# Kernel tuning notes

Hardware: AMD Instinct MI355X
Metric: run time of the kernel (lower is better)

## Reference

```python
import jax, jax.numpy as jnp
import numpy as np

B, T, E, H = 1024, 200, 128, 128
N_ITEMS, N_CATS = 100000, 1000
LN_EPS = 1e-5


def _prelu(x, a):
    return jnp.where(x >= 0, x, a * x)


def _layernorm(x, g, b):
    m = x.mean(-1, keepdims=True)
    v = ((x - m) ** 2).mean(-1, keepdims=True)
    return (x - m) / jnp.sqrt(v + LN_EPS) * g + b


def setup_inputs() -> dict:
    key = jax.random.key(0)
    it = iter(jax.random.split(key, 64))
    nx = lambda: next(it)
    def lin(out_d, in_d):
        s = 1.0 / np.sqrt(in_d)
        return jax.random.uniform(nx(), (out_d, in_d), jnp.float32, -s, s)
    inp = {}
    inp['behavior_ids'] = jax.random.randint(nx(), (B, T), 0, N_ITEMS)
    inp['candidate_id'] = jax.random.randint(nx(), (B,), 0, N_ITEMS)
    inp['candidate_cat'] = jax.random.randint(nx(), (B,), 0, N_CATS)
    inp['dense_features'] = jax.random.normal(nx(), (B, 5), jnp.float32)
    inp['item_emb'] = (jax.random.normal(nx(), (N_ITEMS, E), jnp.float32) * 0.01).at[0].set(0.0)
    inp['cat_emb'] = (jax.random.normal(nx(), (N_CATS, E // 2), jnp.float32) * 0.01).at[0].set(0.0)
    # nn.GRU params (gate order r,z,n)
    inp['gru_wih'] = lin(3 * H, E)
    inp['gru_whh'] = lin(3 * H, H)
    inp['gru_bih'] = jnp.zeros((3 * H,), jnp.float32)
    inp['gru_bhh'] = jnp.zeros((3 * H,), jnp.float32)
    # auxiliary_net: Linear(H,E) -> ReLU -> Linear(E,1)
    inp['aux_w1'] = lin(E, H); inp['aux_b1'] = jnp.zeros((E,), jnp.float32)
    inp['aux_w2'] = lin(1, E); inp['aux_b2'] = jnp.zeros((1,), jnp.float32)
    # attention_mlp: Linear(3H,64) -> PReLU -> Linear(64,1)
    inp['att_w1'] = lin(64, 3 * H); inp['att_b1'] = jnp.zeros((64,), jnp.float32)
    inp['att_a'] = jnp.array(0.25, jnp.float32)
    inp['att_w2'] = lin(1, 64); inp['att_b2'] = jnp.zeros((1,), jnp.float32)
    # AUGRU gates: Linear(2H, H) each
    inp['wz'] = lin(H, 2 * H); inp['bz'] = jnp.zeros((H,), jnp.float32)
    inp['wr'] = lin(H, 2 * H); inp['br'] = jnp.zeros((H,), jnp.float32)
    inp['wh'] = lin(H, 2 * H); inp['bh'] = jnp.zeros((H,), jnp.float32)
    # dense_proj Linear(5,32)
    inp['dp_w'] = lin(32, 5); inp['dp_b'] = jnp.zeros((32,), jnp.float32)
    # MLP: 352 -> 256 -> 128 -> 64, each Linear + LayerNorm + PReLU
    dims = [H + E + E // 2 + 32, 256, 128, 64]
    for i in range(3):
        inp[f'm_w{i+1}'] = lin(dims[i + 1], dims[i])
        inp[f'm_b{i+1}'] = jnp.zeros((dims[i + 1],), jnp.float32)
        inp[f'ln_g{i+1}'] = jnp.ones((dims[i + 1],), jnp.float32)
        inp[f'ln_b{i+1}'] = jnp.zeros((dims[i + 1],), jnp.float32)
        inp[f'pa{i+1}'] = jnp.array(0.25, jnp.float32)
    # 3 task heads Linear(64,1), stacked
    inp['heads_w'] = lin(3, 64); inp['heads_b'] = jnp.zeros((3,), jnp.float32)
    return inp


def _forward_core(behavior_ids, candidate_id, candidate_cat, dense_features,
                  item_emb, cat_emb, gru_wih, gru_whh, gru_bih, gru_bhh,
                  aux_w1, aux_b1, aux_w2, aux_b2,
                  att_w1, att_b1, att_a, att_w2, att_b2,
                  wz, bz, wr, br, wh, bh, dp_w, dp_b,
                  m_w1, m_b1, ln_g1, ln_b1, pa1,
                  m_w2, m_b2, ln_g2, ln_b2, pa2,
                  m_w3, m_b3, ln_g3, ln_b3, pa3,
                  heads_w, heads_b):
    beh = item_emb[behavior_ids]            # [B,T,E]
    cand = item_emb[candidate_id]           # [B,E]
    catv = cat_emb[candidate_cat]           # [B,E//2]
    Bsz = beh.shape[0]
    Hd = gru_whh.shape[1]
    h0 = jnp.zeros((Bsz, Hd), beh.dtype)
    # --- interest extractor GRU (cuDNN GRU math, gate order r,z,n) ---
    xp = jnp.einsum('bte,ge->btg', beh, gru_wih) + gru_bih  # [B,T,3H]
    def gru_step(h, x):
        hp = h @ gru_whh.T + gru_bhh
        xr, xz, xn = jnp.split(x, 3, -1)
        hr, hz, hn = jnp.split(hp, 3, -1)
        r = jax.nn.sigmoid(xr + hr)
        z = jax.nn.sigmoid(xz + hz)
        n = jnp.tanh(xn + r * hn)
        hnew = (1 - z) * n + z * h
        return hnew, hnew
    _, hs = jax.lax.scan(gru_step, h0, jnp.swapaxes(xp, 0, 1))
    hs = jnp.swapaxes(hs, 0, 1)             # [B,T,H]
    # --- auxiliary logits ---
    aux = jax.nn.relu(hs[:, :-1] @ aux_w1.T + aux_b1) @ aux_w2.T + aux_b2  # [B,T-1,1]
    # --- attention (embed_dim == hidden_size so cand_proj == candidate_emb) ---
    ce = cand[:, None, :]
    att_in = jnp.concatenate([hs, jnp.broadcast_to(ce, hs.shape), hs * ce], -1)  # [B,T,3H]
    scores = (_prelu(att_in @ att_w1.T + att_b1, att_a) @ att_w2.T + att_b2)[..., 0]
    att = jax.nn.softmax(scores, axis=-1)   # [B,T]
    # --- AUGRU: attention-modulated update gate ---
    def augru_step(h, xs):
        x, a = xs                           # x: [B,H], a: [B]
        comb = jnp.concatenate([x, h], -1)
        z = jax.nn.sigmoid(comb @ wz.T + bz)
        r = jax.nn.sigmoid(comb @ wr.T + br)
        comb_r = jnp.concatenate([x, r * h], -1)
        ht = jnp.tanh(comb_r @ wh.T + bh)
        zp = a[:, None] * z
        return (1 - zp) * h + zp * ht, None
    hT, _ = jax.lax.scan(augru_step, h0, (jnp.swapaxes(hs, 0, 1), att.T))
    # --- fusion MLP (dropout is identity in eval) ---
    dense_out = dense_features @ dp_w.T + dp_b
    x = jnp.concatenate([hT, cand, catv, dense_out], -1)  # [B,352]
    for (w, b, g, be, a) in ((m_w1, m_b1, ln_g1, ln_b1, pa1),
                             (m_w2, m_b2, ln_g2, ln_b2, pa2),
                             (m_w3, m_b3, ln_g3, ln_b3, pa3)):
        x = _prelu(_layernorm(x @ w.T + b, g, be), a)
    preds = jax.nn.sigmoid(x @ heads_w.T + heads_b)  # [B,3] == 3 heads of [B,1]
    return preds, aux


def reference(behavior_ids, candidate_id, candidate_cat, dense_features,
              item_emb, cat_emb, gru_wih, gru_whh, gru_bih, gru_bhh,
              aux_w1, aux_b1, aux_w2, aux_b2,
              att_w1, att_b1, att_a, att_w2, att_b2,
              wz, bz, wr, br, wh, bh, dp_w, dp_b,
              m_w1, m_b1, ln_g1, ln_b1, pa1,
              m_w2, m_b2, ln_g2, ln_b2, pa2,
              m_w3, m_b3, ln_g3, ln_b3, pa3,
              heads_w, heads_b):
    return _forward_core(behavior_ids, candidate_id, candidate_cat, dense_features,
                         item_emb, cat_emb, gru_wih, gru_whh, gru_bih, gru_bhh,
                         aux_w1, aux_b1, aux_w2, aux_b2,
                         att_w1, att_b1, att_a, att_w2, att_b2,
                         wz, bz, wr, br, wh, bh, dp_w, dp_b,
                         m_w1, m_b1, ln_g1, ln_b1, pa1,
                         m_w2, m_b2, ln_g2, ln_b2, pa2,
                         m_w3, m_b3, ln_g3, ln_b3, pa3,
                         heads_w, heads_b)
```

## Files before the change

kernel.cpp:

```cpp
#include <hip/hip_runtime.h>


typedef __bf16 bf16;
typedef float f32x4 __attribute__((ext_vector_type(4)));
typedef __bf16 bf16x8 __attribute__((ext_vector_type(8)));
typedef __bf16 bf16x4 __attribute__((ext_vector_type(4)));

#define MFMA16(a, b, c) __builtin_amdgcn_mfma_f32_16x16x32_bf16((a), (b), (c), 0, 0, 0)

#define BATCH 1024
#define SEQT 200
#define F32_ONE 0x3F800000u

__device__ __forceinline__ float sigm(float x) {
  return __builtin_amdgcn_rcpf(1.0f + __expf(-x));
}
__device__ __forceinline__ float tanh_fast(float x) {
  float ax = fabsf(x);
  float t = 1.0f - 2.0f * __builtin_amdgcn_rcpf(__expf(2.0f * ax) + 1.0f);
  return copysignf(t, x);
}

__device__ __forceinline__ void bar_lgkm() {
  asm volatile("s_waitcnt lgkmcnt(0)\n\ts_barrier" ::: "memory");
}

__device__ __forceinline__ void dma16(const void* g, void* l) {
  __builtin_amdgcn_global_load_lds((__attribute__((address_space(1))) void*)g,
                                   (__attribute__((address_space(3))) void*)l,
                                   16, 0, 0);
}

template <typename DT> __device__ __forceinline__ float ldf(const DT* p, long i);
template <> __device__ __forceinline__ float ldf<bf16>(const bf16* p, long i) { return (float)p[i]; }
template <> __device__ __forceinline__ float ldf<float>(const float* p, long i) { return p[i]; }

template <typename DT> __device__ __forceinline__ bf16x8 ld8(const DT* p, long i);
template <> __device__ __forceinline__ bf16x8 ld8<bf16>(const bf16* p, long i) {
  return *(const bf16x8*)(p + i);
}
template <> __device__ __forceinline__ bf16x8 ld8<float>(const float* p, long i) {
  f32x4 a = *(const f32x4*)(p + i);
  f32x4 b = *(const f32x4*)(p + i + 4);
  bf16x8 r;
  r[0] = (bf16)a[0]; r[1] = (bf16)a[1]; r[2] = (bf16)a[2]; r[3] = (bf16)a[3];
  r[4] = (bf16)b[0]; r[5] = (bf16)b[1]; r[6] = (bf16)b[2]; r[7] = (bf16)b[3];
  return r;
}

template <typename DT>
__device__ __forceinline__ void prep_body(
    const int* __restrict__ cid, const int* __restrict__ ccat,
    const DT* __restrict__ dense, const DT* __restrict__ item_emb,
    const DT* __restrict__ cat_emb, const DT* __restrict__ dp_w,
    const DT* __restrict__ dp_b, bf16* __restrict__ candbuf, bf16* __restrict__ xf) {
  const int b = blockIdx.x;
  const int t = threadIdx.x;
  bf16 v = (bf16)ldf(item_emb, (long)cid[b] * 128 + t);
  candbuf[b * 128 + t] = v;
  xf[(long)b * 352 + 128 + t] = v;
  if (t < 64) xf[(long)b * 352 + 256 + t] = (bf16)ldf(cat_emb, (long)ccat[b] * 64 + t);
  if (t < 32) {
    float s = ldf(dp_b, t);
    for (int k = 0; k < 5; k++) s += ldf(dense, b * 5 + k) * ldf(dp_w, t * 5 + k);
    xf[(long)b * 352 + 320 + t] = (bf16)s;
  }
}
__global__ __launch_bounds__(128) void k_prep(
    const unsigned* __restrict__ disc, const int* cid, const int* ccat,
    const void* dense, const void* item_emb, const void* cat_emb,
    const void* dp_w, const void* dp_b, bf16* candbuf, bf16* xf) {
  if (*disc == F32_ONE)
    prep_body<float>(cid, ccat, (const float*)dense, (const float*)item_emb,
                     (const float*)cat_emb, (const float*)dp_w, (const float*)dp_b, candbuf, xf);
  else
    prep_body<bf16>(cid, ccat, (const bf16*)dense, (const bf16*)item_emb,
                    (const bf16*)cat_emb, (const bf16*)dp_w, (const bf16*)dp_b, candbuf, xf);
}

template <typename DT>
__device__ __forceinline__ void gru3_body(
    const int* __restrict__ ids, const DT* __restrict__ item_emb,
    const DT* __restrict__ wih, const DT* __restrict__ whh,
    const DT* __restrict__ bih, const DT* __restrict__ bhh, bf16* __restrict__ hs,
    bf16 (*hA)[16][136], bf16 (*xb)[4][16][136], char* raw) {
  const int b0 = blockIdx.x * 16;
  const int tid = threadIdx.x;
  const int w = tid >> 6, lane = tid & 63, l15 = lane & 15, quad = lane >> 4;
  const int nc = w * 16 + l15;

  for (int i = tid; i < 2 * 16 * 136; i += 512) ((bf16*)hA)[i] = (bf16)0.0f;

  bf16x8 wir[4], wiz[4], win_[4], whr[4], whz[4], whn[4];
#pragma unroll
  for (int k = 0; k < 4; k++) {
    const long off = k * 32 + quad * 8;
    wir[k] = ld8(wih, (long)nc * 128 + off);
    wiz[k] = ld8(wih, (long)(128 + nc) * 128 + off);
    win_[k] = ld8(wih, (long)(256 + nc) * 128 + off);
    whr[k] = ld8(whh, (long)nc * 128 + off);
    whz[k] = ld8(whh, (long)(128 + nc) * 128 + off);
    whn[k] = ld8(whh, (long)(256 + nc) * 128 + off);
  }
  const float br_s = ldf(bih, nc) + ldf(bhh, nc);
  const float bz_s = ldf(bih, 128 + nc) + ldf(bhh, 128 + nc);
  const float bxn_s = ldf(bih, 256 + nc);
  const float bhn_s = ldf(bhh, 256 + nc);

  const int idrow = (sizeof(DT) == 4) ? (tid >> 5) : ((tid >> 4) & 15);
  const int* idbase = ids + (long)(b0 + idrow) * SEQT;

  auto DMA = [&](const int4 id4) {
    if constexpr (sizeof(DT) == 4) {
#pragma unroll
      for (int j = 0; j < 4; j++)
        dma16((const char*)(item_emb + (long)((&id4.x)[j]) * 128) + (tid & 31) * 16,
              raw + (j * 512 + tid) * 16);
    } else {
#pragma unroll
      for (int j = 0; j < 2; j++) {
        const int slot = j * 2 + (tid >> 8);
        dma16((const char*)(item_emb + (long)((&id4.x)[slot]) * 128) + (tid & 15) * 16,
              raw + (j * 512 + tid) * 16);
      }
    }
  };
  auto CONV = [&](int buf) {
    if constexpr (sizeof(DT) == 4) {
      const float* rf = (const float*)raw;
#pragma unroll
      for (int h = 0; h < 4; h++) {
        const int e = h * 2048 + tid * 4;
        f32x4 a = *(const f32x4*)(rf + e);
        const int slot = e >> 11, row = (e >> 7) & 15, col = e & 127;
        bf16x4 o;
        o[0] = (bf16)a[0]; o[1] = (bf16)a[1]; o[2] = (bf16)a[2]; o[3] = (bf16)a[3];
        *(bf16x4*)&xb[buf][slot][row][col] = o;
      }
    } else {
      const bf16* rh = (const bf16*)raw;
#pragma unroll
      for (int h = 0; h < 2; h++) {
        const int e = h * 4096 + tid * 8;
        const int slot = e >> 11, row = (e >> 7) & 15, col = e & 127;
        *(bf16x8*)&xb[buf][slot][row][col] = *(const bf16x8*)(rh + e);
      }
    }
  };

  const int srow = tid >> 5, sch = (tid & 31) * 4;
  bf16* hsb = hs + ((long)(b0 + srow) * SEQT) * 128 + sch;

  float hreg[4] = {0.f, 0.f, 0.f, 0.f};
  const f32x4 z4 = {0.f, 0.f, 0.f, 0.f};

  int4 idv = *(const int4*)(idbase);
  DMA(idv);
  idv = *(const int4*)(idbase + 4);
  asm volatile("s_waitcnt vmcnt(1)" ::: "memory");
  __builtin_amdgcn_sched_barrier(0);
  __builtin_amdgcn_s_barrier();
  CONV(0);
  asm volatile("s_waitcnt lgkmcnt(0)" ::: "memory");
  __builtin_amdgcn_sched_barrier(0);
  __builtin_amdgcn_s_barrier();
  DMA(idv);
  idv = *(const int4*)(idbase + 8);

#define GRU_STEP(P, S)                                                         \
  {                                                                            \
    const int tt = t0 + (S);                                                   \
    bf16x8 af[4], xaf[4];                                                      \
    _Pragma("unroll") for (int k = 0; k < 4; k++) {                            \
      af[k] = *(const bf16x8*)&hA[P][l15][k * 32 + quad * 8];                  \
      xaf[k] = *(const bf16x8*)&xb[buf][S][l15][k * 32 + quad * 8];            \
    }                                                                          \
    { const int slot = tt ? tt - 1 : 0;                                        \
      bf16x4 hv = *(const bf16x4*)&hA[P][srow][sch];                           \
      *(bf16x4*)(hsb + (long)slot * 128) = hv; }                               \
    f32x4 ar = z4, az = z4, axn = z4, ahn = z4;                                \
    _Pragma("unroll") for (int k = 0; k < 4; k++) {                            \
      ar = MFMA16(xaf[k], wir[k], ar);                                         \
      az = MFMA16(xaf[k], wiz[k], az);                                         \
      axn = MFMA16(xaf[k], win_[k], axn);                                      \
    }                                                                          \
    _Pragma("unroll") for (int k = 0; k < 4; k++) {                            \
      ar = MFMA16(af[k], whr[k], ar);                                          \
      az = MFMA16(af[k], whz[k], az);                                          \
      ahn = MFMA16(af[k], whn[k], ahn);                                        \
    }                                                                          \
    _Pragma("unroll") for (int r = 0; r < 4; r++) {                            \
      float r_ = sigm(ar[r] + br_s);                                           \
      float z_ = sigm(az[r] + bz_s);                                           \
      float n_ = tanh_fast(axn[r] + bxn_s + r_ * (ahn[r] + bhn_s));            \
      float hnew = (1.0f - z_) * n_ + z_ * hreg[r];                            \
      hreg[r] = hnew;                                                          \
      hA[(P) ^ 1][quad * 4 + r][nc] = (bf16)hnew;                              \
    }                                                                          \
    bar_lgkm();                                                                \
  }

  for (int c = 0; c < 50; c++) {
    const int t0 = c * 4;
    const int buf = c & 1;
    GRU_STEP(0, 0) GRU_STEP(1, 1) GRU_STEP(0, 2) GRU_STEP(1, 3)
    if (c < 49) {
      asm volatile("s_waitcnt vmcnt(4)" ::: "memory");
      __builtin_amdgcn_sched_barrier(0);
      __builtin_amdgcn_s_barrier();
      CONV((c + 1) & 1);
      asm volatile("s_waitcnt lgkmcnt(0)" ::: "memory");
      __builtin_amdgcn_sched_barrier(0);
      __builtin_amdgcn_s_barrier();
      if (c < 48) {
        DMA(idv);
        int nid = (c + 3) * 4; if (nid > 196) nid = 196;
        idv = *(const int4*)(idbase + nid);
      }
    }
  }
#undef GRU_STEP
  { bf16x4 hv = *(const bf16x4*)&hA[0][srow][sch];
    *(bf16x4*)(hsb + (long)(SEQT - 1) * 128) = hv; }
}
__global__ __launch_bounds__(512, 1) void k_gru3(
    const unsigned* __restrict__ disc, const int* ids, const void* item_emb,
    const void* wih, const void* whh, const void* bih, const void* bhh, bf16* hs) {
  __shared__ __align__(16) bf16 hA[2][16][136];
  __shared__ __align__(16) bf16 xb[2][4][16][136];
  __shared__ __align__(16) char raw[32768];
  if (*disc == F32_ONE)
    gru3_body<float>(ids, (const float*)item_emb, (const float*)wih, (const float*)whh,
                     (const float*)bih, (const float*)bhh, hs, hA, xb, raw);
  else
    gru3_body<bf16>(ids, (const bf16*)item_emb, (const bf16*)wih, (const bf16*)whh,
                    (const bf16*)bih, (const bf16*)bhh, hs, hA, xb, raw);
}

template <typename DT>
__device__ __forceinline__ void augru3_body(
    const bf16* __restrict__ hsrc, const float* __restrict__ att,
    const DT* __restrict__ wz, const DT* __restrict__ wr, const DT* __restrict__ wh,
    const DT* __restrict__ bzv, const DT* __restrict__ brv, const DT* __restrict__ bhv,
    bf16* __restrict__ xf_out,
    bf16 (*hA)[16][136], bf16 (*rhA)[136], float (*attL)[201],
    bf16 (*xb)[4][16][136], char* raw) {
  const int b0 = blockIdx.x * 16;
  const int tid = threadIdx.x;
  const int w = tid >> 6, lane = tid & 63, l15 = lane & 15, quad = lane >> 4;
  const int nc = w * 16 + l15;

  for (int i = tid; i < 2 * 16 * 136; i += 512) ((bf16*)hA)[i] = (bf16)0.0f;
  for (int i = tid; i < 16 * SEQT; i += 512) {
    int r = i / SEQT, c = i - r * SEQT;
    attL[r][c] = att[(long)(b0 + r) * SEQT + c];
  }

  bf16x8 wzx[4], wzh[4], wrx[4], wrh[4], whx[4], whh_[4];
#pragma unroll
  for (int k = 0; k < 4; k++) {
    const long off = k * 32 + quad * 8;
    wzx[k] = ld8(wz, (long)nc * 256 + off);
    wzh[k] = ld8(wz, (long)nc * 256 + 128 + off);
    wrx[k] = ld8(wr, (long)nc * 256 + off);
    wrh[k] = ld8(wr, (long)nc * 256 + 128 + off);
    whx[k] = ld8(wh, (long)nc * 256 + off);
    whh_[k] = ld8(wh, (long)nc * 256 + 128 + off);
  }
  const float bz_s = ldf(bzv, nc);
  const float br_s = ldf(brv, nc);
  const float bh_s = ldf(bhv, nc);

  auto DMA = [&](int t0) {
#pragma unroll
    for (int j = 0; j < 2; j++) {
      const int slot = j * 2 + (tid >> 8);
      const int row = (tid >> 4) & 15;
      const bf16* src = hsrc + ((long)(b0 + row) * SEQT + t0 + slot) * 128 + (tid & 15) * 8;
      dma16(src, raw + (j * 512 + tid) * 16);
    }
  };
  auto CONV = [&](int buf) {
    const bf16* rh = (const bf16*)raw;
#pragma unroll
    for (int h = 0; h < 2; h++) {
      const int e = h * 4096 + tid * 8;
      const int slot = e >> 11, row = (e >> 7) & 15, col = e & 127;
      *(bf16x8*)&xb[buf][slot][row][col] = *(const bf16x8*)(rh + e);
    }
  };

  float hreg[4] = {0.f, 0.f, 0.f, 0.f};
  const f32x4 z4 = {0.f, 0.f, 0.f, 0.f};

  DMA(0);
  asm volatile("s_waitcnt vmcnt(0)" ::: "memory");
  __builtin_amdgcn_sched_barrier(0);
  __builtin_amdgcn_s_barrier();
  CONV(0);
  asm volatile("s_waitcnt lgkmcnt(0)" ::: "memory");
  __builtin_amdgcn_sched_barrier(0);
  __builtin_amdgcn_s_barrier();
  DMA(4);

#define AUGRU_STEP(P, S)                                                       \
  {                                                                            \
    const int tt = t0 + (S);                                                   \
    bf16x8 af[4], xaf[4];                                                      \
    _Pragma("unroll") for (int k = 0; k < 4; k++) {                            \
      af[k] = *(const bf16x8*)&hA[P][l15][k * 32 + quad * 8];                  \
      xaf[k] = *(const bf16x8*)&xb[buf][S][l15][k * 32 + quad * 8];            \
    }                                                                          \
    f32x4 az = z4, ar = z4, axh = z4;                                          \
    _Pragma("unroll") for (int k = 0; k < 4; k++) {                            \
      az = MFMA16(xaf[k], wzx[k], az);                                         \
      ar = MFMA16(xaf[k], wrx[k], ar);                                         \
      axh = MFMA16(xaf[k], whx[k], axh);                                       \
    }                                                                          \
    _Pragma("unroll") for (int k = 0; k < 4; k++) {                            \
      az = MFMA16(af[k], wzh[k], az);                                          \
      ar = MFMA16(af[k], wrh[k], ar);                                          \
    }                                                                          \
    float zp[4];                                                               \
    _Pragma("unroll") for (int r = 0; r < 4; r++) {                            \
      float a_ = attL[quad * 4 + r][tt];                                       \
      float z_ = sigm(az[r] + bz_s);                                           \
      float r_ = sigm(ar[r] + br_s);                                           \
      zp[r] = a_ * z_;                                                         \
      rhA[quad * 4 + r][nc] = (bf16)(r_ * hreg[r]);                            \
    }                                                                          \
    bar_lgkm();                                                                \
    bf16x8 rf[4];                                                              \
    _Pragma("unroll") for (int k = 0; k < 4; k++)                              \
      rf[k] = *(const bf16x8*)&rhA[l15][k * 32 + quad * 8];                    \
    f32x4 ahh = axh;                                                           \
    _Pragma("unroll") for (int k = 0; k < 4; k++)                              \
      ahh = MFMA16(rf[k], whh_[k], ahh);                                       \
    _Pragma("unroll") for (int r = 0; r < 4; r++) {                            \
      float ht = tanh_fast(ahh[r] + bh_s);                                     \
      float hnew = (1.f - zp[r]) * hreg[r] + zp[r] * ht;                       \
      hreg[r] = hnew;                                                          \
      hA[(P) ^ 1][quad * 4 + r][nc] = (bf16)hnew;                              \
    }                                                                          \
    bar_lgkm();                                                                \
  }

  for (int c = 0; c < 50; c++) {
    const int t0 = c * 4;
    const int buf = c & 1;
    AUGRU_STEP(0, 0) AUGRU_STEP(1, 1) AUGRU_STEP(0, 2) AUGRU_STEP(1, 3)
    if (c < 49) {
      asm volatile("s_waitcnt vmcnt(0)" ::: "memory");
      __builtin_amdgcn_sched_barrier(0);
      __builtin_amdgcn_s_barrier();
      CONV((c + 1) & 1);
      asm volatile("s_waitcnt lgkmcnt(0)" ::: "memory");
      __builtin_amdgcn_sched_barrier(0);
      __builtin_amdgcn_s_barrier();
      if (c < 48) DMA((c + 2) * 4);
    }
  }
#undef AUGRU_STEP
#pragma unroll
  for (int r = 0; r < 4; r++)
    xf_out[(long)(b0 + quad * 4 + r) * 352 + nc] = (bf16)hreg[r];
}
__global__ __launch_bounds__(512, 1) void k_augru3(
    const unsigned* __restrict__ disc, const bf16* hsrc, const float* att,
    const void* wz, const void* wr, const void* wh,
    const void* bzv, const void* brv, const void* bhv, bf16* xf_out) {
  __shared__ __align__(16) bf16 hA[2][16][136];
  __shared__ __align__(16) bf16 rhA[16][136];
  __shared__ __align__(16) float attL[16][201];
  __shared__ __align__(16) bf16 xb[2][4][16][136];
  __shared__ __align__(16) char raw[16384];
  if (*disc == F32_ONE)
    augru3_body<float>(hsrc, att, (const float*)wz, (const float*)wr, (const float*)wh,
                       (const float*)bzv, (const float*)brv, (const float*)bhv, xf_out,
                       hA, rhA, attL, xb, raw);
  else
    augru3_body<bf16>(hsrc, att, (const bf16*)wz, (const bf16*)wr, (const bf16*)wh,
                      (const bf16*)bzv, (const bf16*)brv, (const bf16*)bhv, xf_out,
                      hA, rhA, attL, xb, raw);
}

template <typename DT>
__device__ __forceinline__ void aux_body(
    const bf16* __restrict__ hs, const DT* __restrict__ w1, const DT* __restrict__ b1v,
    const DT* __restrict__ w2v, const DT* __restrict__ b2v, float* __restrict__ outaux,
    bf16 (*As)[136], bf16 (*Ws)[136]) {
  const int bg = blockIdx.y;
  const int t0 = blockIdx.x * 64;
  const int tid = threadIdx.x;
  const int w = tid >> 6, lane = tid & 63, l15 = lane & 15, quad = lane >> 4;
#pragma unroll
  for (int j = 0; j < 8; j++) {
    int ci = j * 256 + tid;
    int row = ci >> 4, k8 = (ci & 15) * 8;
    *(bf16x8*)&Ws[row][k8] = ld8(w1, (long)row * 128 + k8);
  }
  float b1c[8], w2c[8];
#pragma unroll
  for (int nt = 0; nt < 8; nt++) {
    int n = nt * 16 + l15;
    b1c[nt] = ldf(b1v, n);
    w2c[nt] = ldf(w2v, n);
  }
  const float b2 = ldf(b2v, 0);
  const f32x4 z4 = {0.f, 0.f, 0.f, 0.f};
  __syncthreads();

  for (int bi = 0; bi < 16; bi++) {
    const int b = bg * 16 + bi;
#pragma unroll
    for (int j = 0; j < 4; j++) {
      int ci = j * 256 + tid;
      int row = ci >> 4, k8 = (ci & 15) * 8;
      int t = t0 + row; int tc = t < 199 ? t : 198;
      *(bf16x8*)&As[row][k8] = *(const bf16x8*)(hs + ((long)b * SEQT + tc) * 128 + k8);
    }
    bar_lgkm();
    bf16x8 af[4];
#pragma unroll
    for (int k = 0; k < 4; k++) af[k] = *(const bf16x8*)&As[w * 16 + l15][k * 32 + quad * 8];
    float part[4] = {0.f, 0.f, 0.f, 0.f};
#pragma unroll
    for (int nt = 0; nt < 8; nt++) {
      f32x4 acc = z4;
#pragma unroll
      for (int k = 0; k < 4; k++) {
        bf16x8 bfr = *(const bf16x8*)&Ws[nt * 16 + l15][k * 32 + quad * 8];
        acc = MFMA16(af[k], bfr, acc);
      }
#pragma unroll
      for (int r = 0; r < 4; r++) {
        float y = acc[r] + b1c[nt];
        part[r] += (y > 0.f ? y : 0.f) * w2c[nt];
      }
    }
#pragma unroll
    for (int m = 1; m < 16; m <<= 1)
#pragma unroll
      for (int r = 0; r < 4; r++) part[r] += __shfl_xor(part[r], m, 64);
    if (l15 == 0) {
#pragma unroll
      for (int r = 0; r < 4; r++) {
        int t = t0 + w * 16 + quad * 4 + r;
        if (t < 199) outaux[(long)b * 199 + t] = part[r] + b2;
      }
    }
    bar_lgkm();
  }
}
__global__ __launch_bounds__(256) void k_aux(
    const unsigned* __restrict__ disc, const bf16* hs, const void* w1, const void* b1v,
    const void* w2v, const void* b2v, float* outaux) {
  __shared__ bf16 As[64][136];
  __shared__ bf16 Ws[128][136];
  if (*disc == F32_ONE)
    aux_body<float>(hs, (const float*)w1, (const float*)b1v, (const float*)w2v,
                    (const float*)b2v, outaux, As, Ws);
  else
    aux_body<bf16>(hs, (const bf16*)w1, (const bf16*)b1v, (const bf16*)w2v,
                   (const bf16*)b2v, outaux, As, Ws);
}

template <typename DT>
__device__ __forceinline__ void att_body(
    const bf16* __restrict__ hs, const bf16* __restrict__ cand,
    const DT* __restrict__ w1, const DT* __restrict__ b1v, const DT* __restrict__ a_s,
    const DT* __restrict__ w2v, const DT* __restrict__ b2v, float* __restrict__ scores,
    bf16 (*As)[392], bf16 (*Ws)[392]) {
  const int bg = blockIdx.y;
  const int t0 = blockIdx.x * 64;
  const int tid = threadIdx.x;
  const int w = tid >> 6, lane = tid & 63, l15 = lane & 15, quad = lane >> 4;
#pragma unroll
  for (int j = 0; j < 12; j++) {
    int ci = j * 256 + tid;
    int row = ci / 48;
    int k8 = (ci % 48) * 8;
    *(bf16x8*)&Ws[row][k8] = ld8(w1, (long)row * 384 + k8);
  }
  const float aP = ldf(a_s, 0);
  const float b2 = ldf(b2v, 0);
  float b1c[4], w2c[4];
#pragma unroll
  for (int nt = 0; nt < 4; nt++) {
    int n = nt * 16 + l15;
    b1c[nt] = ldf(b1v, n);
    w2c[nt] = ldf(w2v, n);
  }
  const f32x4 z4 = {0.f, 0.f, 0.f, 0.f};
  __syncthreads();

  for (int bi = 0; bi < 16; bi++) {
    const int b = bg * 16 + bi;
#pragma unroll
    for (int j = 0; j < 12; j++) {
      int ci = j * 256 + tid;
      int row = ci / 48;
      int k8 = (ci % 48) * 8;
      int t = t0 + row; int tc = t < SEQT ? t : SEQT - 1;
      const bf16* hrow = hs + ((long)b * SEQT + tc) * 128;
      bf16x8 v;
      if (k8 < 128) v = *(const bf16x8*)(hrow + k8);
      else if (k8 < 256) v = *(const bf16x8*)(cand + b * 128 + (k8 - 128));
      else {
        bf16x8 hv = *(const bf16x8*)(hrow + (k8 - 256));
        bf16x8 cv = *(const bf16x8*)(cand + b * 128 + (k8 - 256));
#pragma unroll
        for (int q = 0; q < 8; q++) v[q] = (bf16)((float)hv[q] * (float)cv[q]);
      }
      *(bf16x8*)&As[row][k8] = v;
    }
    bar_lgkm();
    f32x4 acc[4] = {z4, z4, z4, z4};
    for (int k = 0; k < 12; k++) {
      bf16x8 af = *(const bf16x8*)&As[w * 16 + l15][k * 32 + quad * 8];
#pragma unroll
      for (int nt = 0; nt < 4; nt++) {
        bf16x8 bfr = *(const bf16x8*)&Ws[nt * 16 + l15][k * 32 + quad * 8];
        acc[nt] = MFMA16(af, bfr, acc[nt]);
      }
    }
    float part[4] = {0.f, 0.f, 0.f, 0.f};
#pragma unroll
    for (int nt = 0; nt < 4; nt++) {
#pragma unroll
      for (int r = 0; r < 4; r++) {
        float y = acc[nt][r] + b1c[nt];
        y = (y >= 0.f) ? y : aP * y;
        part[r] += y * w2c[nt];
      }
    }
#pragma unroll
    for (int m = 1; m < 16; m <<= 1)
#pragma unroll
      for (int r = 0; r < 4; r++) part[r] += __shfl_xor(part[r], m, 64);
    if (l15 == 0) {
#pragma unroll
      for (int r = 0; r < 4; r++) {
        int t = t0 + w * 16 + quad * 4 + r;
        if (t < SEQT) scores[(long)b * SEQT + t] = part[r] + b2;
      }
    }
    bar_lgkm();
  }
}
__global__ __launch_bounds__(256) void k_att(
    const unsigned* __restrict__ disc, const bf16* hs, const bf16* cand,
    const void* w1, const void* b1v, const void* a_s,
    const void* w2v, const void* b2v, float* scores) {
  __shared__ bf16 As[64][392];
  __shared__ bf16 Ws[64][392];
  if (*disc == F32_ONE)
    att_body<float>(hs, cand, (const float*)w1, (const float*)b1v, (const float*)a_s,
                    (const float*)w2v, (const float*)b2v, scores, As, Ws);
  else
    att_body<bf16>(hs, cand, (const bf16*)w1, (const bf16*)b1v, (const bf16*)a_s,
                   (const bf16*)w2v, (const bf16*)b2v, scores, As, Ws);
}

__global__ __launch_bounds__(256) void k_softmax(float* __restrict__ sc) {
  const int b = blockIdx.x, tid = threadIdx.x;
  __shared__ float red[256];
  float v = (tid < SEQT) ? sc[(long)b * SEQT + tid] : -1e30f;
  red[tid] = v; __syncthreads();
  for (int s = 128; s > 0; s >>= 1) { if (tid < s) red[tid] = fmaxf(red[tid], red[tid + s]); __syncthreads(); }
  float mx = red[0]; __syncthreads();
  float e = (tid < SEQT) ? __expf(v - mx) : 0.f;
  red[tid] = e; __syncthreads();
  for (int s = 128; s > 0; s >>= 1) { if (tid < s) red[tid] += red[tid + s]; __syncthreads(); }
  float inv = 1.0f / red[0];
  if (tid < SEQT) sc[(long)b * SEQT + tid] = e * inv;
}

template <typename DT>
__device__ __forceinline__ void mlp_body(
    const bf16* __restrict__ xf,
    const DT* __restrict__ w1, const DT* __restrict__ b1, const DT* __restrict__ g1, const DT* __restrict__ be1, const DT* __restrict__ pa1,
    const DT* __restrict__ w2, const DT* __restrict__ b2, const DT* __restrict__ g2, const DT* __restrict__ be2, const DT* __restrict__ pa2,
    const DT* __restrict__ w3, const DT* __restrict__ b3, const DT* __restrict__ g3, const DT* __restrict__ be3, const DT* __restrict__ pa3,
    const DT* __restrict__ hw, const DT* __restrict__ hb, float* __restrict__ preds,
    float (*xs)[352], float (*ys)[256]) {
  const int tid = threadIdx.x, w = tid >> 6, lane = tid & 63;
  const int b = blockIdx.x * 4 + w;
  for (int i = lane; i < 352; i += 64) xs[w][i] = (float)xf[(long)b * 352 + i];
  __syncthreads();
  float acc1[4];
#pragma unroll
  for (int oi = 0; oi < 4; oi++) {
    int o = lane + 64 * oi;
    float s = ldf(b1, o);
    for (int k = 0; k < 352; k += 8) {
      bf16x8 wv = ld8(w1, (long)o * 352 + k);
#pragma unroll
      for (int j = 0; j < 8; j++) s += xs[w][k + j] * (float)wv[j];
    }
    acc1[oi] = s;
  }
  float sm = acc1[0] + acc1[1] + acc1[2] + acc1[3];
#pragma unroll
  for (int m = 1; m < 64; m <<= 1) sm += __shfl_xor(sm, m, 64);
  float mean = sm * (1.0f / 256.0f);
  float vs = 0.f;
#pragma unroll
  for (int oi = 0; oi < 4; oi++) { float d = acc1[oi] - mean; vs += d * d; }
#pragma unroll
  for (int m = 1; m < 64; m <<= 1) vs += __shfl_xor(vs, m, 64);
  float rstd = rsqrtf(vs * (1.0f / 256.0f) + 1e-5f);
  float a1 = ldf(pa1, 0);
#pragma unroll
  for (int oi = 0; oi < 4; oi++) {
    int o = lane + 64 * oi;
    float y = (acc1[oi] - mean) * rstd * ldf(g1, o) + ldf(be1, o);
    ys[w][o] = (y >= 0.f) ? y : a1 * y;
  }
  __syncthreads();
  float acc2[2];
#pragma unroll
  for (int oi = 0; oi < 2; oi++) {
    int o = lane + 64 * oi;
    float s = ldf(b2, o);
    for (int k = 0; k < 256; k += 8) {
      bf16x8 wv = ld8(w2, (long)o * 256 + k);
#pragma unroll
      for (int j = 0; j < 8; j++) s += ys[w][k + j] * (float)wv[j];
    }
    acc2[oi] = s;
  }
  sm = acc2[0] + acc2[1];
#pragma unroll
  for (int m = 1; m < 64; m <<= 1) sm += __shfl_xor(sm, m, 64);
  mean = sm * (1.0f / 128.0f);
  vs = 0.f;
#pragma unroll
  for (int oi = 0; oi < 2; oi++) { float d = acc2[oi] - mean; vs += d * d; }
#pragma unroll
  for (int m = 1; m < 64; m <<= 1) vs += __shfl_xor(vs, m, 64);
  rstd = rsqrtf(vs * (1.0f / 128.0f) + 1e-5f);
  float a2 = ldf(pa2, 0);
  __syncthreads();
#pragma unroll
  for (int oi = 0; oi < 2; oi++) {
    int o = lane + 64 * oi;
    float y = (acc2[oi] - mean) * rstd * ldf(g2, o) + ldf(be2, o);
    xs[w][o] = (y >= 0.f) ? y : a2 * y;
  }
  __syncthreads();
  float s3 = ldf(b3, lane);
  for (int k = 0; k < 128; k += 8) {
    bf16x8 wv = ld8(w3, (long)lane * 128 + k);
#pragma unroll
    for (int j = 0; j < 8; j++) s3 += xs[w][k + j] * (float)wv[j];
  }
  sm = s3;
#pragma unroll
  for (int m = 1; m < 64; m <<= 1) sm += __shfl_xor(sm, m, 64);
  mean = sm * (1.0f / 64.0f);
  float d3 = s3 - mean;
  vs = d3 * d3;
#pragma unroll
  for (int m = 1; m < 64; m <<= 1) vs += __shfl_xor(vs, m, 64);
  rstd = rsqrtf(vs * (1.0f / 64.0f) + 1e-5f);
  float a3 = ldf(pa3, 0);
  float y3 = d3 * rstd * ldf(g3, lane) + ldf(be3, lane);
  y3 = (y3 >= 0.f) ? y3 : a3 * y3;
  ys[w][lane] = y3;
  __syncthreads();
  if (lane < 3) {
    float s = ldf(hb, lane);
    for (int k = 0; k < 64; k++) s += ys[w][k] * ldf(hw, lane * 64 + k);
    preds[(long)b * 3 + lane] = sigm(s);
  }
}
__global__ __launch_bounds__(256) void k_mlp(
    const unsigned* __restrict__ disc, const bf16* xf,
    const void* w1, const void* b1, const void* g1, const void* be1, const void* pa1,
    const void* w2, const void* b2, const void* g2, const void* be2, const void* pa2,
    const void* w3, const void* b3, const void* g3, const void* be3, const void* pa3,
    const void* hw, const void* hb, float* preds) {
  __shared__ float xs[4][352];
  __shared__ float ys[4][256];
  if (*disc == F32_ONE)
    mlp_body<float>(xf,
        (const float*)w1, (const float*)b1, (const float*)g1, (const float*)be1, (const float*)pa1,
        (const float*)w2, (const float*)b2, (const float*)g2, (const float*)be2, (const float*)pa2,
        (const float*)w3, (const float*)b3, (const float*)g3, (const float*)be3, (const float*)pa3,
        (const float*)hw, (const float*)hb, preds, xs, ys);
  else
    mlp_body<bf16>(xf,
        (const bf16*)w1, (const bf16*)b1, (const bf16*)g1, (const bf16*)be1, (const bf16*)pa1,
        (const bf16*)w2, (const bf16*)b2, (const bf16*)g2, (const bf16*)be2, (const bf16*)pa2,
        (const bf16*)w3, (const bf16*)b3, (const bf16*)g3, (const bf16*)be3, (const bf16*)pa3,
        (const bf16*)hw, (const bf16*)hb, preds, xs, ys);
}

extern "C" void kernel_launch(void* const* d_in, const int* in_sizes, int n_in,
                              void* d_out, int out_size, void* d_ws, size_t ws_size,
                              hipStream_t stream) {
  const int* behavior_ids = (const int*)d_in[0];
  const int* candidate_id = (const int*)d_in[1];
  const int* candidate_cat = (const int*)d_in[2];
  const void* dense = d_in[3];
  const void* item_emb = d_in[4];
  const void* cat_emb = d_in[5];
  const void* gru_wih = d_in[6];
  const void* gru_whh = d_in[7];
  const void* gru_bih = d_in[8];
  const void* gru_bhh = d_in[9];
  const void* aux_w1 = d_in[10];
  const void* aux_b1 = d_in[11];
  const void* aux_w2 = d_in[12];
  const void* aux_b2 = d_in[13];
  const void* att_w1 = d_in[14];
  const void* att_b1 = d_in[15];
  const void* att_a = d_in[16];
  const void* att_w2 = d_in[17];
  const void* att_b2 = d_in[18];
  const void* wz = d_in[19];
  const void* bz = d_in[20];
  const void* wr = d_in[21];
  const void* br = d_in[22];
  const void* wh = d_in[23];
  const void* bh = d_in[24];
  const void* dp_w = d_in[25];
  const void* dp_b = d_in[26];
  const void* m_w1 = d_in[27];
  const void* m_b1 = d_in[28];
  const void* ln_g1 = d_in[29];
  const void* ln_b1 = d_in[30];
  const void* pa1 = d_in[31];
  const void* m_w2 = d_in[32];
  const void* m_b2 = d_in[33];
  const void* ln_g2 = d_in[34];
  const void* ln_b2 = d_in[35];
  const void* pa2 = d_in[36];
  const void* m_w3 = d_in[37];
  const void* m_b3 = d_in[38];
  const void* ln_g3 = d_in[39];
  const void* ln_b3 = d_in[40];
  const void* pa3 = d_in[41];
  const void* heads_w = d_in[42];
  const void* heads_b = d_in[43];
  (void)in_sizes; (void)n_in; (void)out_size; (void)ws_size;

  const unsigned* disc = (const unsigned*)ln_g1;

  char* ws = (char*)d_ws;
  bf16* HS = (bf16*)(ws);
  float* SC = (float*)(ws + 52428800L);
  bf16* CAND = (bf16*)(ws + 53248000L);
  bf16* XF = (bf16*)(ws + 53510144L);
  float* OUT = (float*)d_out;

  k_prep<<<BATCH, 128, 0, stream>>>(disc, candidate_id, candidate_cat, dense, item_emb,
                                    cat_emb, dp_w, dp_b, CAND, XF);
  k_gru3<<<64, 512, 0, stream>>>(disc, behavior_ids, item_emb, gru_wih, gru_whh,
                                 gru_bih, gru_bhh, HS);
  k_aux<<<dim3(4, 64), 256, 0, stream>>>(disc, HS, aux_w1, aux_b1, aux_w2, aux_b2, OUT + 3072);
  k_att<<<dim3(4, 64), 256, 0, stream>>>(disc, HS, CAND, att_w1, att_b1, att_a, att_w2, att_b2, SC);
  k_softmax<<<BATCH, 256, 0, stream>>>(SC);
  k_augru3<<<64, 512, 0, stream>>>(disc, HS, SC, wz, wr, wh, bz, br, bh, XF);
  k_mlp<<<256, 256, 0, stream>>>(disc, XF,
      m_w1, m_b1, ln_g1, ln_b1, pa1,
      m_w2, m_b2, ln_g2, ln_b2, pa2,
      m_w3, m_b3, ln_g3, ln_b3, pa3,
      heads_w, heads_b, OUT);
}
```

Before: 831.4 us.

## Fuse prep, aux, attention and softmax into one heads kernel

```diff
diff --git a/kernel.cpp b/kernel.cpp
--- a/kernel.cpp
+++ b/kernel.cpp
@@ -46,36 +46,6 @@
   r[0] = (bf16)a[0]; r[1] = (bf16)a[1]; r[2] = (bf16)a[2]; r[3] = (bf16)a[3];
   r[4] = (bf16)b[0]; r[5] = (bf16)b[1]; r[6] = (bf16)b[2]; r[7] = (bf16)b[3];
   return r;
-}
-
-template <typename DT>
-__device__ __forceinline__ void prep_body(
-    const int* __restrict__ cid, const int* __restrict__ ccat,
-    const DT* __restrict__ dense, const DT* __restrict__ item_emb,
-    const DT* __restrict__ cat_emb, const DT* __restrict__ dp_w,
-    const DT* __restrict__ dp_b, bf16* __restrict__ candbuf, bf16* __restrict__ xf) {
-  const int b = blockIdx.x;
-  const int t = threadIdx.x;
-  bf16 v = (bf16)ldf(item_emb, (long)cid[b] * 128 + t);
-  candbuf[b * 128 + t] = v;
-  xf[(long)b * 352 + 128 + t] = v;
-  if (t < 64) xf[(long)b * 352 + 256 + t] = (bf16)ldf(cat_emb, (long)ccat[b] * 64 + t);
-  if (t < 32) {
-    float s = ldf(dp_b, t);
-    for (int k = 0; k < 5; k++) s += ldf(dense, b * 5 + k) * ldf(dp_w, t * 5 + k);
-    xf[(long)b * 352 + 320 + t] = (bf16)s;
-  }
-}
-__global__ __launch_bounds__(128) void k_prep(
-    const unsigned* __restrict__ disc, const int* cid, const int* ccat,
-    const void* dense, const void* item_emb, const void* cat_emb,
-    const void* dp_w, const void* dp_b, bf16* candbuf, bf16* xf) {
-  if (*disc == F32_ONE)
-    prep_body<float>(cid, ccat, (const float*)dense, (const float*)item_emb,
-                     (const float*)cat_emb, (const float*)dp_w, (const float*)dp_b, candbuf, xf);
-  else
-    prep_body<bf16>(cid, ccat, (const bf16*)dense, (const bf16*)item_emb,
-                    (const bf16*)cat_emb, (const bf16*)dp_w, (const bf16*)dp_b, candbuf, xf);
 }
 
 template <typename DT>
@@ -238,6 +208,165 @@
 }
 
 template <typename DT>
+__device__ __forceinline__ void heads_body(
+    const bf16* __restrict__ hs,
+    const int* __restrict__ cid, const int* __restrict__ ccat,
+    const DT* __restrict__ dense, const DT* __restrict__ item_emb,
+    const DT* __restrict__ cat_emb, const DT* __restrict__ dp_w, const DT* __restrict__ dp_b,
+    const DT* __restrict__ aw1, const DT* __restrict__ ab1,
+    const DT* __restrict__ aw2, const DT* __restrict__ ab2,
+    const DT* __restrict__ tw1, const DT* __restrict__ tb1, const DT* __restrict__ ta,
+    const DT* __restrict__ tw2, const DT* __restrict__ tb2,
+    float* __restrict__ sc, float* __restrict__ outaux, bf16* __restrict__ xf,
+    bf16 (*Wt)[392], bf16 (*Wa)[136], float (*scL)[208]) {
+  const int bg = blockIdx.x, b0 = bg * 16;
+  const int tid = threadIdx.x, w = tid >> 6, lane = tid & 63, l15 = lane & 15, quad = lane >> 4;
+
+  for (int i = tid; i < 64 * 48; i += 512) {
+    int row = i / 48, k8 = (i % 48) * 8;
+    *(bf16x8*)&Wt[row][k8] = ld8(tw1, (long)row * 384 + k8);
+  }
+  for (int i = tid; i < 128 * 16; i += 512) {
+    int row = i >> 4, k8 = (i & 15) * 8;
+    *(bf16x8*)&Wa[row][k8] = ld8(aw1, (long)row * 128 + k8);
+  }
+  for (int i = tid; i < 16 * 128; i += 512) {
+    int b = b0 + (i >> 7), c = i & 127;
+    xf[(long)b * 352 + 128 + c] = (bf16)ldf(item_emb, (long)cid[b] * 128 + c);
+  }
+  for (int i = tid; i < 16 * 64; i += 512) {
+    int b = b0 + (i >> 6), c = i & 63;
+    xf[(long)b * 352 + 256 + c] = (bf16)ldf(cat_emb, (long)ccat[b] * 64 + c);
+  }
+  if (tid < 16 * 32) {
+    int b = b0 + (tid >> 5), c = tid & 31;
+    float s = ldf(dp_b, c);
+    for (int k = 0; k < 5; k++) s += ldf(dense, b * 5 + k) * ldf(dp_w, c * 5 + k);
+    xf[(long)b * 352 + 320 + c] = (bf16)s;
+  }
+  bf16x8 candf[4];
+#pragma unroll
+  for (int k = 0; k < 4; k++)
+    candf[k] = ld8(item_emb, (long)cid[b0 + l15] * 128 + k * 32 + quad * 8);
+  float tb1c[4], tw2c[4], ab1c[8], aw2c[8];
+#pragma unroll
+  for (int nt = 0; nt < 4; nt++) { tb1c[nt] = ldf(tb1, nt * 16 + l15); tw2c[nt] = ldf(tw2, nt * 16 + l15); }
+#pragma unroll
+  for (int nt = 0; nt < 8; nt++) { ab1c[nt] = ldf(ab1, nt * 16 + l15); aw2c[nt] = ldf(aw2, nt * 16 + l15); }
+  const float aP = ldf(ta, 0), tb2s = ldf(tb2, 0), ab2s = ldf(ab2, 0);
+  __syncthreads();
+
+  const f32x4 z4 = {0.f, 0.f, 0.f, 0.f};
+  bf16x8 af[4], afn[4];
+  {
+    const int t = w;
+#pragma unroll
+    for (int k = 0; k < 4; k++)
+      af[k] = *(const bf16x8*)(hs + ((long)(b0 + l15) * SEQT + t) * 128 + k * 32 + quad * 8);
+  }
+  for (int i = 0; i < 25; i++) {
+    const int t = w + 8 * i;
+    if (i + 1 < 25) {
+      const int tn = t + 8;
+#pragma unroll
+      for (int k = 0; k < 4; k++)
+        afn[k] = *(const bf16x8*)(hs + ((long)(b0 + l15) * SEQT + tn) * 128 + k * 32 + quad * 8);
+    }
+    bf16x8 hcf[4];
+#pragma unroll
+    for (int k = 0; k < 4; k++)
+#pragma unroll
+      for (int j = 0; j < 8; j++) hcf[k][j] = (bf16)((float)af[k][j] * (float)candf[k][j]);
+    float tpart[4] = {0.f, 0.f, 0.f, 0.f};
+#pragma unroll
+    for (int nt = 0; nt < 4; nt++) {
+      f32x4 acc = z4;
+      const bf16* wrow = &Wt[nt * 16 + l15][0];
+#pragma unroll
+      for (int k = 0; k < 4; k++) acc = MFMA16(af[k], *(const bf16x8*)(wrow + k * 32 + quad * 8), acc);
+#pragma unroll
+      for (int k = 0; k < 4; k++) acc = MFMA16(candf[k], *(const bf16x8*)(wrow + 128 + k * 32 + quad * 8), acc);
+#pragma unroll
+      for (int k = 0; k < 4; k++) acc = MFMA16(hcf[k], *(const bf16x8*)(wrow + 256 + k * 32 + quad * 8), acc);
+#pragma unroll
+      for (int r = 0; r < 4; r++) {
+        float y = acc[r] + tb1c[nt];
+        y = (y >= 0.f) ? y : aP * y;
+        tpart[r] += y * tw2c[nt];
+      }
+    }
+    float apart[4] = {0.f, 0.f, 0.f, 0.f};
+#pragma unroll
+    for (int nt = 0; nt < 8; nt++) {
+      f32x4 acc = z4;
+      const bf16* wrow = &Wa[nt * 16 + l15][0];
+#pragma unroll
+      for (int k = 0; k < 4; k++) acc = MFMA16(af[k], *(const bf16x8*)(wrow + k * 32 + quad * 8), acc);
+#pragma unroll
+      for (int r = 0; r < 4; r++) {
+        float y = acc[r] + ab1c[nt];
+        apart[r] += (y > 0.f ? y : 0.f) * aw2c[nt];
+      }
+    }
+#pragma unroll
+    for (int m = 1; m < 16; m <<= 1)
+#pragma unroll
+      for (int r = 0; r < 4; r++) {
+        tpart[r] += __shfl_xor(tpart[r], m, 64);
+        apart[r] += __shfl_xor(apart[r], m, 64);
+      }
+    if (l15 == 0) {
+#pragma unroll
+      for (int r = 0; r < 4; r++) {
+        scL[quad * 4 + r][t] = tpart[r] + tb2s;
+        if (t < SEQT - 1) outaux[(long)(b0 + quad * 4 + r) * 199 + t] = apart[r] + ab2s;
+      }
+    }
+    if (i + 1 < 25) {
+#pragma unroll
+      for (int k = 0; k < 4; k++) af[k] = afn[k];
+    }
+  }
+  __syncthreads();
+  {
+    const int row = tid >> 5, lt = tid & 31;
+    float mx = -1e30f;
+    for (int t = lt; t < SEQT; t += 32) mx = fmaxf(mx, scL[row][t]);
+#pragma unroll
+    for (int m = 1; m < 32; m <<= 1) mx = fmaxf(mx, __shfl_xor(mx, m, 32));
+    float sum = 0.f;
+    for (int t = lt; t < SEQT; t += 32) { float e = __expf(scL[row][t] - mx); scL[row][t] = e; sum += e; }
+#pragma unroll
+    for (int m = 1; m < 32; m <<= 1) sum += __shfl_xor(sum, m, 32);
+    float inv = 1.0f / sum;
+    for (int t = lt; t < SEQT; t += 32) sc[(long)(b0 + row) * SEQT + t] = scL[row][t] * inv;
+  }
+}
+__global__ __launch_bounds__(512, 1) void k_heads(
+    const unsigned* __restrict__ disc, const bf16* hs,
+    const int* cid, const int* ccat, const void* dense, const void* item_emb,
+    const void* cat_emb, const void* dp_w, const void* dp_b,
+    const void* aw1, const void* ab1, const void* aw2, const void* ab2,
+    const void* tw1, const void* tb1, const void* ta, const void* tw2, const void* tb2,
+    float* sc, float* outaux, bf16* xf) {
+  __shared__ __align__(16) bf16 Wt[64][392];
+  __shared__ __align__(16) bf16 Wa[128][136];
+  __shared__ __align__(16) float scL[16][208];
+  if (*disc == F32_ONE)
+    heads_body<float>(hs, cid, ccat, (const float*)dense, (const float*)item_emb,
+                      (const float*)cat_emb, (const float*)dp_w, (const float*)dp_b,
+                      (const float*)aw1, (const float*)ab1, (const float*)aw2, (const float*)ab2,
+                      (const float*)tw1, (const float*)tb1, (const float*)ta,
+                      (const float*)tw2, (const float*)tb2, sc, outaux, xf, Wt, Wa, scL);
+  else
+    heads_body<bf16>(hs, cid, ccat, (const bf16*)dense, (const bf16*)item_emb,
+                     (const bf16*)cat_emb, (const bf16*)dp_w, (const bf16*)dp_b,
+                     (const bf16*)aw1, (const bf16*)ab1, (const bf16*)aw2, (const bf16*)ab2,
+                     (const bf16*)tw1, (const bf16*)tb1, (const bf16*)ta,
+                     (const bf16*)tw2, (const bf16*)tb2, sc, outaux, xf, Wt, Wa, scL);
+}
+
+template <typename DT>
 __device__ __forceinline__ void augru3_body(
     const bf16* __restrict__ hsrc, const float* __restrict__ att,
     const DT* __restrict__ wz, const DT* __restrict__ wr, const DT* __restrict__ wh,
@@ -385,198 +514,6 @@
 }
 
 template <typename DT>
-__device__ __forceinline__ void aux_body(
-    const bf16* __restrict__ hs, const DT* __restrict__ w1, const DT* __restrict__ b1v,
-    const DT* __restrict__ w2v, const DT* __restrict__ b2v, float* __restrict__ outaux,
-    bf16 (*As)[136], bf16 (*Ws)[136]) {
-  const int bg = blockIdx.y;
-  const int t0 = blockIdx.x * 64;
-  const int tid = threadIdx.x;
-  const int w = tid >> 6, lane = tid & 63, l15 = lane & 15, quad = lane >> 4;
-#pragma unroll
-  for (int j = 0; j < 8; j++) {
-    int ci = j * 256 + tid;
-    int row = ci >> 4, k8 = (ci & 15) * 8;
-    *(bf16x8*)&Ws[row][k8] = ld8(w1, (long)row * 128 + k8);
-  }
-  float b1c[8], w2c[8];
-#pragma unroll
-  for (int nt = 0; nt < 8; nt++) {
-    int n = nt * 16 + l15;
-    b1c[nt] = ldf(b1v, n);
-    w2c[nt] = ldf(w2v, n);
-  }
-  const float b2 = ldf(b2v, 0);
-  const f32x4 z4 = {0.f, 0.f, 0.f, 0.f};
-  __syncthreads();
-
-  for (int bi = 0; bi < 16; bi++) {
-    const int b = bg * 16 + bi;
-#pragma unroll
-    for (int j = 0; j < 4; j++) {
-      int ci = j * 256 + tid;
-      int row = ci >> 4, k8 = (ci & 15) * 8;
-      int t = t0 + row; int tc = t < 199 ? t : 198;
-      *(bf16x8*)&As[row][k8] = *(const bf16x8*)(hs + ((long)b * SEQT + tc) * 128 + k8);
-    }
-    bar_lgkm();
-    bf16x8 af[4];
-#pragma unroll
-    for (int k = 0; k < 4; k++) af[k] = *(const bf16x8*)&As[w * 16 + l15][k * 32 + quad * 8];
-    float part[4] = {0.f, 0.f, 0.f, 0.f};
-#pragma unroll
-    for (int nt = 0; nt < 8; nt++) {
-      f32x4 acc = z4;
-#pragma unroll
-      for (int k = 0; k < 4; k++) {
-        bf16x8 bfr = *(const bf16x8*)&Ws[nt * 16 + l15][k * 32 + quad * 8];
-        acc = MFMA16(af[k], bfr, acc);
-      }
-#pragma unroll
-      for (int r = 0; r < 4; r++) {
-        float y = acc[r] + b1c[nt];
-        part[r] += (y > 0.f ? y : 0.f) * w2c[nt];
-      }
-    }
-#pragma unroll
-    for (int m = 1; m < 16; m <<= 1)
-#pragma unroll
-      for (int r = 0; r < 4; r++) part[r] += __shfl_xor(part[r], m, 64);
-    if (l15 == 0) {
-#pragma unroll
-      for (int r = 0; r < 4; r++) {
-        int t = t0 + w * 16 + quad * 4 + r;
-        if (t < 199) outaux[(long)b * 199 + t] = part[r] + b2;
-      }
-    }
-    bar_lgkm();
-  }
-}
-__global__ __launch_bounds__(256) void k_aux(
-    const unsigned* __restrict__ disc, const bf16* hs, const void* w1, const void* b1v,
-    const void* w2v, const void* b2v, float* outaux) {
-  __shared__ bf16 As[64][136];
-  __shared__ bf16 Ws[128][136];
-  if (*disc == F32_ONE)
-    aux_body<float>(hs, (const float*)w1, (const float*)b1v, (const float*)w2v,
-                    (const float*)b2v, outaux, As, Ws);
-  else
-    aux_body<bf16>(hs, (const bf16*)w1, (const bf16*)b1v, (const bf16*)w2v,
-                   (const bf16*)b2v, outaux, As, Ws);
-}
-
-template <typename DT>
-__device__ __forceinline__ void att_body(
-    const bf16* __restrict__ hs, const bf16* __restrict__ cand,
-    const DT* __restrict__ w1, const DT* __restrict__ b1v, const DT* __restrict__ a_s,
-    const DT* __restrict__ w2v, const DT* __restrict__ b2v, float* __restrict__ scores,
-    bf16 (*As)[392], bf16 (*Ws)[392]) {
-  const int bg = blockIdx.y;
-  const int t0 = blockIdx.x * 64;
-  const int tid = threadIdx.x;
-  const int w = tid >> 6, lane = tid & 63, l15 = lane & 15, quad = lane >> 4;
-#pragma unroll
-  for (int j = 0; j < 12; j++) {
-    int ci = j * 256 + tid;
-    int row = ci / 48;
-    int k8 = (ci % 48) * 8;
-    *(bf16x8*)&Ws[row][k8] = ld8(w1, (long)row * 384 + k8);
-  }
-  const float aP = ldf(a_s, 0);
-  const float b2 = ldf(b2v, 0);
-  float b1c[4], w2c[4];
-#pragma unroll
-  for (int nt = 0; nt < 4; nt++) {
-    int n = nt * 16 + l15;
-    b1c[nt] = ldf(b1v, n);
-    w2c[nt] = ldf(w2v, n);
-  }
-  const f32x4 z4 = {0.f, 0.f, 0.f, 0.f};
-  __syncthreads();
-
-  for (int bi = 0; bi < 16; bi++) {
-    const int b = bg * 16 + bi;
-#pragma unroll
-    for (int j = 0; j < 12; j++) {
-      int ci = j * 256 + tid;
-      int row = ci / 48;
-      int k8 = (ci % 48) * 8;
-      int t = t0 + row; int tc = t < SEQT ? t : SEQT - 1;
-      const bf16* hrow = hs + ((long)b * SEQT + tc) * 128;
-      bf16x8 v;
-      if (k8 < 128) v = *(const bf16x8*)(hrow + k8);
-      else if (k8 < 256) v = *(const bf16x8*)(cand + b * 128 + (k8 - 128));
-      else {
-        bf16x8 hv = *(const bf16x8*)(hrow + (k8 - 256));
-        bf16x8 cv = *(const bf16x8*)(cand + b * 128 + (k8 - 256));
-#pragma unroll
-        for (int q = 0; q < 8; q++) v[q] = (bf16)((float)hv[q] * (float)cv[q]);
-      }
-      *(bf16x8*)&As[row][k8] = v;
-    }
-    bar_lgkm();
-    f32x4 acc[4] = {z4, z4, z4, z4};
-    for (int k = 0; k < 12; k++) {
-      bf16x8 af = *(const bf16x8*)&As[w * 16 + l15][k * 32 + quad * 8];
-#pragma unroll
-      for (int nt = 0; nt < 4; nt++) {
-        bf16x8 bfr = *(const bf16x8*)&Ws[nt * 16 + l15][k * 32 + quad * 8];
-        acc[nt] = MFMA16(af, bfr, acc[nt]);
-      }
-    }
-    float part[4] = {0.f, 0.f, 0.f, 0.f};
-#pragma unroll
-    for (int nt = 0; nt < 4; nt++) {
-#pragma unroll
-      for (int r = 0; r < 4; r++) {
-        float y = acc[nt][r] + b1c[nt];
-        y = (y >= 0.f) ? y : aP * y;
-        part[r] += y * w2c[nt];
-      }
-    }
-#pragma unroll
-    for (int m = 1; m < 16; m <<= 1)
-#pragma unroll
-      for (int r = 0; r < 4; r++) part[r] += __shfl_xor(part[r], m, 64);
-    if (l15 == 0) {
-#pragma unroll
-      for (int r = 0; r < 4; r++) {
-        int t = t0 + w * 16 + quad * 4 + r;
-        if (t < SEQT) scores[(long)b * SEQT + t] = part[r] + b2;
-      }
-    }
-    bar_lgkm();
-  }
-}
-__global__ __launch_bounds__(256) void k_att(
-    const unsigned* __restrict__ disc, const bf16* hs, const bf16* cand,
-    const void* w1, const void* b1v, const void* a_s,
-    const void* w2v, const void* b2v, float* scores) {
-  __shared__ bf16 As[64][392];
-  __shared__ bf16 Ws[64][392];
-  if (*disc == F32_ONE)
-    att_body<float>(hs, cand, (const float*)w1, (const float*)b1v, (const float*)a_s,
-                    (const float*)w2v, (const float*)b2v, scores, As, Ws);
-  else
-    att_body<bf16>(hs, cand, (const bf16*)w1, (const bf16*)b1v, (const bf16*)a_s,
-                   (const bf16*)w2v, (const bf16*)b2v, scores, As, Ws);
-}
-
-__global__ __launch_bounds__(256) void k_softmax(float* __restrict__ sc) {
-  const int b = blockIdx.x, tid = threadIdx.x;
-  __shared__ float red[256];
-  float v = (tid < SEQT) ? sc[(long)b * SEQT + tid] : -1e30f;
-  red[tid] = v; __syncthreads();
-  for (int s = 128; s > 0; s >>= 1) { if (tid < s) red[tid] = fmaxf(red[tid], red[tid + s]); __syncthreads(); }
-  float mx = red[0]; __syncthreads();
-  float e = (tid < SEQT) ? __expf(v - mx) : 0.f;
-  red[tid] = e; __syncthreads();
-  for (int s = 128; s > 0; s >>= 1) { if (tid < s) red[tid] += red[tid + s]; __syncthreads(); }
-  float inv = 1.0f / red[0];
-  if (tid < SEQT) sc[(long)b * SEQT + tid] = e * inv;
-}
-
-template <typename DT>
 __device__ __forceinline__ void mlp_body(
     const bf16* __restrict__ xf,
     const DT* __restrict__ w1, const DT* __restrict__ b1, const DT* __restrict__ g1, const DT* __restrict__ be1, const DT* __restrict__ pa1,
@@ -585,7 +522,7 @@
     const DT* __restrict__ hw, const DT* __restrict__ hb, float* __restrict__ preds,
     float (*xs)[352], float (*ys)[256]) {
   const int tid = threadIdx.x, w = tid >> 6, lane = tid & 63;
-  const int b = blockIdx.x * 4 + w;
+  const int b = blockIdx.x * 8 + w;
   for (int i = lane; i < 352; i += 64) xs[w][i] = (float)xf[(long)b * 352 + i];
   __syncthreads();
   float acc1[4];
@@ -675,14 +612,14 @@
     preds[(long)b * 3 + lane] = sigm(s);
   }
 }
-__global__ __launch_bounds__(256) void k_mlp(
+__global__ __launch_bounds__(512) void k_mlp(
     const unsigned* __restrict__ disc, const bf16* xf,
     const void* w1, const void* b1, const void* g1, const void* be1, const void* pa1,
     const void* w2, const void* b2, const void* g2, const void* be2, const void* pa2,
     const void* w3, const void* b3, const void* g3, const void* be3, const void* pa3,
     const void* hw, const void* hb, float* preds) {
-  __shared__ float xs[4][352];
-  __shared__ float ys[4][256];
+  __shared__ float xs[8][352];
+  __shared__ float ys[8][256];
   if (*disc == F32_ONE)
     mlp_body<float>(xf,
         (const float*)w1, (const float*)b1, (const float*)g1, (const float*)be1, (const float*)pa1,
@@ -751,19 +688,18 @@
   char* ws = (char*)d_ws;
   bf16* HS = (bf16*)(ws);
   float* SC = (float*)(ws + 52428800L);
-  bf16* CAND = (bf16*)(ws + 53248000L);
   bf16* XF = (bf16*)(ws + 53510144L);
   float* OUT = (float*)d_out;
 
-  k_prep<<<BATCH, 128, 0, stream>>>(disc, candidate_id, candidate_cat, dense, item_emb,
-                                    cat_emb, dp_w, dp_b, CAND, XF);
   k_gru3<<<64, 512, 0, stream>>>(disc, behavior_ids, item_emb, gru_wih, gru_whh,
                                  gru_bih, gru_bhh, HS);
-  k_aux<<<dim3(4, 64), 256, 0, stream>>>(disc, HS, aux_w1, aux_b1, aux_w2, aux_b2, OUT + 3072);
-  k_att<<<dim3(4, 64), 256, 0, stream>>>(disc, HS, CAND, att_w1, att_b1, att_a, att_w2, att_b2, SC);
-  k_softmax<<<BATCH, 256, 0, stream>>>(SC);
+  k_heads<<<64, 512, 0, stream>>>(disc, HS, candidate_id, candidate_cat, dense,
+                                  item_emb, cat_emb, dp_w, dp_b,
+                                  aux_w1, aux_b1, aux_w2, aux_b2,
+                                  att_w1, att_b1, att_a, att_w2, att_b2,
+                                  SC, OUT + 3072, XF);
   k_augru3<<<64, 512, 0, stream>>>(disc, HS, SC, wz, wr, wh, bz, br, bh, XF);
-  k_mlp<<<256, 256, 0, stream>>>(disc, XF,
+  k_mlp<<<128, 512, 0, stream>>>(disc, XF,
       m_w1, m_b1, ln_g1, ln_b1, pa1,
       m_w2, m_b2, ln_g2, ln_b2, pa2,
       m_w3, m_b3, ln_g3, ln_b3, pa3,
```

Result: slower. 1.050 ms (+26.3%).
